# Performance work log

Hardware: AMD Instinct MI355X
Metric: run time of the kernel (lower is better)

The kernel has to match this reference:

```python
import jax, jax.numpy as jnp
import numpy as np

B, S, T = 1024, 1024, 16


def setup_inputs() -> dict:
    key = jax.random.key(0)
    k1, k2, k3, k4, k5 = jax.random.split(key, 5)
    emissions = jax.random.normal(k1, (B, S, T), dtype=jnp.float32)
    tags = jax.random.randint(k2, (B, S), 0, T, dtype=jnp.int64)
    mask = jnp.ones((B, S), dtype=bool)
    # parameters (original uses uniform(-0.1, 0.1) init)
    transitions = jax.random.uniform(k3, (T, T), minval=-0.1, maxval=0.1, dtype=jnp.float32)
    start_transitions = jax.random.uniform(k4, (T,), minval=-0.1, maxval=0.1, dtype=jnp.float32)
    end_transitions = jax.random.uniform(k5, (T,), minval=-0.1, maxval=0.1, dtype=jnp.float32)
    return {
        "emissions": emissions,
        "tags": tags,
        "mask": mask,
        "transitions": transitions,
        "start_transitions": start_transitions,
        "end_transitions": end_transitions,
    }


def _forward_algorithm(emissions, mask, transitions, start_transitions, end_transitions):
    # emissions: [B,S,T], mask: [B,S] bool -> log partition [B]
    score0 = start_transitions + emissions[:, 0]  # [B,T]

    def step(score, xs):
        em_t, m_t = xs  # em_t: [B,T], m_t: [B]
        # next[b,i,j] = score[b,i] + transitions[i,j] + em_t[b,j]
        nxt = score[:, :, None] + transitions[None, :, :] + em_t[:, None, :]
        nxt = jax.nn.logsumexp(nxt, axis=1)  # over previous tag i
        score = jnp.where(m_t[:, None], nxt, score)
        return score, None

    em_rest = jnp.swapaxes(emissions[:, 1:], 0, 1)  # [S-1,B,T]
    m_rest = jnp.swapaxes(mask[:, 1:], 0, 1)        # [S-1,B]
    score, _ = jax.lax.scan(step, score0, (em_rest, m_rest))
    score = score + end_transitions
    return jax.nn.logsumexp(score, axis=1)


def _score_sentence(emissions, tags, mask, transitions, start_transitions, end_transitions):
    # gold-path score, vectorized over time. [B]
    bidx = jnp.arange(emissions.shape[0])
    score = start_transitions[tags[:, 0]] + emissions[:, 0][bidx, tags[:, 0]]
    # per-step emission scores [B,S]
    emit = jnp.take_along_axis(emissions, tags[:, :, None], axis=2)[:, :, 0]
    # NOTE: faithful to original: transitions[tags[t], tags[t-1]]
    trans = transitions[tags[:, 1:], tags[:, :-1]]  # [B,S-1]
    m = mask[:, 1:].astype(emissions.dtype)
    score = score + jnp.sum((emit[:, 1:] + trans) * m, axis=1)
    last_idx = jnp.sum(mask.astype(jnp.int32), axis=1) - 1  # [B]
    last_tags = jnp.take_along_axis(tags, last_idx[:, None].astype(tags.dtype), axis=1)[:, 0]
    score = score + end_transitions[last_tags]
    return score


def reference(emissions, tags, mask, transitions, start_transitions, end_transitions):
    emissions = emissions.astype(jnp.float32)
    gold = _score_sentence(emissions, tags, mask, transitions, start_transitions, end_transitions)
    logZ = _forward_algorithm(emissions, mask, transitions, start_transitions, end_transitions)
    nll = logZ - gold
    return jnp.mean(nll)
```

## Files before the change

### kernel.cpp

```cpp
#include <hip/hip_runtime.h>
#include <stdint.h>


#define BB 1024
#define SS 1024
#define TT 16
#define WPB 8
#define TL  128
#define XS  68
#define MS  20
#define OFFLN2 3.29244911f

typedef float    f32x4 __attribute__((ext_vector_type(4)));
typedef float    f32x2 __attribute__((ext_vector_type(2)));
typedef int      i32x4 __attribute__((ext_vector_type(4)));
typedef short    s16x8 __attribute__((ext_vector_type(8)));
typedef uint32_t u32x4 __attribute__((ext_vector_type(4)));

__device__ __forceinline__ uint32_t pkt(float lo, float hi) {
    return __builtin_amdgcn_perm(__float_as_uint(hi), __float_as_uint(lo), 0x07060302u);
}

#define RESCALE(sd, sc) {                                                   \
        float mx_ = fmaxf(fmaxf(sd[0], sd[1]), fmaxf(sd[2], sd[3]));        \
        mx_ = fmaxf(mx_, __shfl_xor(mx_, 16, 64));                          \
        mx_ = fmaxf(mx_, __shfl_xor(mx_, 32, 64));                          \
        const int e_ = (int)(__float_as_uint(mx_) >> 23) - 127;             \
        const float sf_ = __uint_as_float((uint32_t)(127 - e_) << 23);      \
        sd[0] *= sf_; sd[1] *= sf_; sd[2] *= sf_; sd[3] *= sf_;             \
        sc += e_; }

__device__ __forceinline__ void run_chains(float* xt, const f32x2 e01, const f32x2 e23,
                                           const int q, const int m, const bool skip_first,
                                           f32x4& P, int& sc)
{
    const f32x4 zero = {0.f, 0.f, 0.f, 0.f};
    f32x4 sd0, sd1;
    sd0[0] = sd1[0] = (4*q + 0 == m) ? 1.f : 0.f;
    sd0[1] = sd1[1] = (4*q + 1 == m) ? 1.f : 0.f;
    sd0[2] = sd1[2] = (4*q + 2 == m) ? 1.f : 0.f;
    sd0[3] = sd1[3] = (4*q + 3 == m) ? 1.f : 0.f;
    u32x4 au0, au1, bu0, bu1;
    au0.z = au0.w = au1.z = au1.w = 0u;
    bu0.z = bu0.w = bu1.z = bu1.w = 0u;

    const float* xr0 = xt + m * XS;
    const float* xr1 = xr0 + 32;

    #pragma unroll
    for (int g = 0; g < 8; ++g) {
        const f32x4 c0 = *(const f32x4*)(xr0 + 4 * g);
        const f32x4 c1 = *(const f32x4*)(xr1 + 4 * g);
        #pragma unroll
        for (int i = 0; i < 4; ++i) {
            if (!(skip_first && g == 0 && i == 0)) {
                f32x2 xx; xx.x = c0[i]; xx.y = c0[i];
                const f32x2 a01 = xx * e01;
                const f32x2 a23 = xx * e23;
                au0.x = pkt(a01.x, a01.y); au0.y = pkt(a23.x, a23.y);
                bu0.x = pkt(sd0[0], sd0[1]); bu0.y = pkt(sd0[2], sd0[3]);
                sd0 = __builtin_amdgcn_mfma_f32_16x16x32_bf16(
                        __builtin_bit_cast(s16x8, au0), __builtin_bit_cast(s16x8, bu0),
                        zero, 0, 0, 0);
            }
            {
                f32x2 xx; xx.x = c1[i]; xx.y = c1[i];
                const f32x2 a01 = xx * e01;
                const f32x2 a23 = xx * e23;
                au1.x = pkt(a01.x, a01.y); au1.y = pkt(a23.x, a23.y);
                bu1.x = pkt(sd1[0], sd1[1]); bu1.y = pkt(sd1[2], sd1[3]);
                sd1 = __builtin_amdgcn_mfma_f32_16x16x32_bf16(
                        __builtin_bit_cast(s16x8, au1), __builtin_bit_cast(s16x8, bu1),
                        zero, 0, 0, 0);
            }
        }
    }

    xt[(4*q + 0) * TT + m] = sd1[0];
    xt[(4*q + 1) * TT + m] = sd1[1];
    xt[(4*q + 2) * TT + m] = sd1[2];
    xt[(4*q + 3) * TT + m] = sd1[3];
    const f32x4 at = *(const f32x4*)(xt + m * TT + 4 * q);
    au0.x = pkt(at.x, at.y);   au0.y = pkt(at.z, at.w);
    bu0.x = pkt(sd0[0], sd0[1]); bu0.y = pkt(sd0[2], sd0[3]);
    P = __builtin_amdgcn_mfma_f32_16x16x32_bf16(
            __builtin_bit_cast(s16x8, au0), __builtin_bit_cast(s16x8, bu0), zero, 0, 0, 0);
    sc = 0;
    RESCALE(P, sc);
}

__global__ __launch_bounds__(512, 8) void crf_fused(
        const float* __restrict__ em,
        const float* __restrict__ trans,
        const int*   __restrict__ tags,
        const float* __restrict__ startt,
        const float* __restrict__ endt,
        float* __restrict__ part)
{
    __shared__ __align__(16) float xbuf[WPB][TT * XS];
    __shared__ __align__(16) int   scb [WPB][16];
    __shared__ float gpart[WPB];

    const int w    = threadIdx.x >> 6;
    const int lane = threadIdx.x & 63;
    const int b    = blockIdx.x;
    const int q    = lane >> 4;
    const int m    = lane & 15;

    const float comp = 1.00390625f;
    f32x2 e01, e23;
    e01.x = __expf(trans[(4*q + 0) * TT + m]) * comp;
    e01.y = __expf(trans[(4*q + 1) * TT + m]) * comp;
    e23.x = __expf(trans[(4*q + 2) * TT + m]) * comp;
    e23.y = __expf(trans[(4*q + 3) * TT + m]) * comp;

    float* xt = xbuf[w];
    const float* ep = em + (size_t)b * SS * TT + (size_t)w * TL * TT + lane;

    {
        float v[16];
        #pragma unroll
        for (int k = 0; k < 16; ++k) v[k] = ep[k * 64];
        #pragma unroll
        for (int k = 0; k < 16; ++k) xt[m * XS + 4 * k + q] = __expf(v[k] - OFFLN2);
    }

    {
        const int t0  = w * TL + lane;
        const int t1  = t0 + 64;
        const int tg0 = tags[b * SS + t0];
        const int tg1 = tags[b * SS + t1];
        float g0 = em[((size_t)b * SS + t0) * TT + tg0];
        float g1 = em[((size_t)b * SS + t1) * TT + tg1];
        g0 += (t0 > 0) ? trans[tg0 * TT + tags[b * SS + t0 - 1]] : startt[tg0];
        g1 += trans[tg1 * TT + tags[b * SS + t1 - 1]];
        if (t1 == SS - 1) g1 += endt[tg1];
        float gs = g0 + g1;
        #pragma unroll
        for (int s2 = 1; s2 < 64; s2 <<= 1) gs += __shfl_xor(gs, s2, 64);
        if (lane == 0) gpart[w] = gs;
    }

    f32x4 PA; int scA;
    run_chains(xt, e01, e23, q, m, (w == 0), PA, scA);

    {
        float v[16];
        #pragma unroll
        for (int k = 0; k < 16; ++k) v[k] = ep[(16 + k) * 64];
        #pragma unroll
        for (int k = 0; k < 16; ++k) xt[m * XS + 4 * k + q] = __expf(v[k] - OFFLN2);
    }
    f32x4 PB; int scB;
    run_chains(xt, e01, e23, q, m, false, PB, scB);

    const f32x4 zero = {0.f, 0.f, 0.f, 0.f};
    xt[(4*q + 0) * TT + m] = PB[0];
    xt[(4*q + 1) * TT + m] = PB[1];
    xt[(4*q + 2) * TT + m] = PB[2];
    xt[(4*q + 3) * TT + m] = PB[3];
    const f32x4 at = *(const f32x4*)(xt + m * TT + 4 * q);
    u32x4 au, bu;
    au.z = au.w = bu.z = bu.w = 0u;
    au.x = pkt(at.x, at.y);   au.y = pkt(at.z, at.w);
    bu.x = pkt(PA[0], PA[1]); bu.y = pkt(PA[2], PA[3]);
    f32x4 sdw = __builtin_amdgcn_mfma_f32_16x16x32_bf16(
            __builtin_bit_cast(s16x8, au), __builtin_bit_cast(s16x8, bu), zero, 0, 0, 0);
    int scw = scA + scB;
    RESCALE(sdw, scw);

    xt[(4*q + 0) * MS + m] = sdw[0];
    xt[(4*q + 1) * MS + m] = sdw[1];
    xt[(4*q + 2) * MS + m] = sdw[2];
    xt[(4*q + 3) * MS + m] = sdw[3];
    if (q == 0) scb[w][m] = scw;
    __syncthreads();

    f32x4 d = zero; int sig = 0;
    #pragma unroll
    for (int lev = 0; lev < 3; ++lev) {
        const int nact = 4 >> lev;
        if (w < nact) {
            const int iA = (2 * w + 1) << lev;
            const int iB = (2 * w) << lev;
            const float* xA = xbuf[iA];
            float*       xB = xbuf[iB];
            const f32x4 a  = *(const f32x4*)(xA + m * MS + 4 * q);
            const i32x4 s4 = *(const i32x4*)(&scb[iA][4 * q]);
            const int   sB = scb[iB][m];
            int smax = max(max(s4.x, s4.y), max(s4.z, s4.w));
            smax = max(smax, __shfl_xor(smax, 16, 64));
            smax = max(smax, __shfl_xor(smax, 32, 64));
            const float bb0 = xB[(4*q + 0) * MS + m];
            const float bb1 = xB[(4*q + 1) * MS + m];
            const float bb2 = xB[(4*q + 2) * MS + m];
            const float bb3 = xB[(4*q + 3) * MS + m];
            const float u0 = ldexpf(bb0, s4.x - smax);
            const float u1 = ldexpf(bb1, s4.y - smax);
            const float u2 = ldexpf(bb2, s4.z - smax);
            const float u3 = ldexpf(bb3, s4.w - smax);
            u32x4 ta, tb;
            ta.z = ta.w = tb.z = tb.w = 0u;
            ta.x = pkt(a.x, a.y); ta.y = pkt(a.z, a.w);
            tb.x = pkt(u0, u1);   tb.y = pkt(u2, u3);
            f32x4 dd = __builtin_amdgcn_mfma_f32_16x16x32_bf16(
                    __builtin_bit_cast(s16x8, ta), __builtin_bit_cast(s16x8, tb), zero, 0, 0, 0);
            int sc_ = sB + smax;
            RESCALE(dd, sc_);
            if (lev == 2) { d = dd; sig = sc_; }
            else {
                xB[(4*q + 0) * MS + m] = dd[0];
                xB[(4*q + 1) * MS + m] = dd[1];
                xB[(4*q + 2) * MS + m] = dd[2];
                xB[(4*q + 3) * MS + m] = dd[3];
                if (q == 0) scb[iB][m] = sc_;
            }
        }
        if (lev < 2) __syncthreads();
    }

    if (w == 0) {
        const float s0 = startt[m] + em[(size_t)b * SS * TT + m];
        float mx0 = s0;
        #pragma unroll
        for (int s2 = 1; s2 < 16; s2 <<= 1) mx0 = fmaxf(mx0, __shfl_xor(mx0, s2, 64));
        const float u0n = __expf(s0 - mx0);
        int sigmax = sig;
        #pragma unroll
        for (int s2 = 1; s2 < 16; s2 <<= 1) sigmax = max(sigmax, __shfl_xor(sigmax, s2, 64));
        const float wt = ldexpf(u0n, sig - sigmax);
        f32x4 v;
        v[0] = d[0] * wt; v[1] = d[1] * wt; v[2] = d[2] * wt; v[3] = d[3] * wt;
        #pragma unroll
        for (int s2 = 1; s2 < 16; s2 <<= 1) {
            v[0] += __shfl_xor(v[0], s2, 64);
            v[1] += __shfl_xor(v[1], s2, 64);
            v[2] += __shfl_xor(v[2], s2, 64);
            v[3] += __shfl_xor(v[3], s2, 64);
        }
        const f32x4 ee = *(const f32x4*)(endt + 4 * q);
        float z = __expf(ee.x) * v[0] + __expf(ee.y) * v[1]
                + __expf(ee.z) * v[2] + __expf(ee.w) * v[3];
        z += __shfl_xor(z, 16, 64);
        z += __shfl_xor(z, 32, 64);
        if (lane == 0) {
            float gb = 0.f;
            #pragma unroll
            for (int i = 0; i < WPB; ++i) gb += gpart[i];
            part[b] = mx0 + 0.69314718055994531f * (float)sigmax
                    + 1023.0f * OFFLN2 + __logf(z) - gb;
        }
    }
}

__global__ __launch_bounds__(256) void reduce_kernel(const float* __restrict__ part,
                                                     float* __restrict__ out)
{
    __shared__ float red[256];
    const int tid = threadIdx.x;
    float s = 0.f;
    #pragma unroll
    for (int i = 0; i < 4; ++i) s += part[tid + 256 * i];
    red[tid] = s;
    __syncthreads();
    for (int k = 128; k > 0; k >>= 1) {
        if (tid < k) red[tid] += red[tid + k];
        __syncthreads();
    }
    if (tid == 0) out[0] = red[0] * (1.0f / BB);
}

extern "C" void kernel_launch(void* const* d_in, const int* in_sizes, int n_in,
                              void* d_out, int out_size, void* d_ws, size_t ws_size,
                              hipStream_t stream) {
    const float* em     = (const float*)d_in[0];
    const int*   tags   = (const int*)  d_in[1];
    const float* trans  = (const float*)d_in[3];
    const float* startt = (const float*)d_in[4];
    const float* endt   = (const float*)d_in[5];
    float* out  = (float*)d_out;
    float* part = (float*)d_ws;

    crf_fused<<<BB, 512, 0, stream>>>(em, trans, tags, startt, endt, part);
    reduce_kernel<<<1, 256, 0, stream>>>(part, out);
}
```

Before: 125.9 us.

## Use four parallel chains with constant MFMA A operand and post-multiply emissions

Restructures the per-warp chain product from two chains of 32 steps to four chains of 16 steps. The exp(transitions) A operand is packed once into a constant bf16 register instead of being rescaled and repacked by the emission column every step. Emissions are now applied by an elementwise multiply on the MFMA output, read from a transposed LDS layout. More independent chains hide MFMA latency, and the per-step packing work shrinks. The cost is two extra matrix merges per phase and a different LDS layout.

```diff
diff --git a/kernel.cpp b/kernel.cpp
--- a/kernel.cpp
+++ b/kernel.cpp
@@ -7,12 +7,10 @@
 #define TT 16
 #define WPB 8
 #define TL  128
-#define XS  68
 #define MS  20
 #define OFFLN2 3.29244911f
 
 typedef float    f32x4 __attribute__((ext_vector_type(4)));
-typedef float    f32x2 __attribute__((ext_vector_type(2)));
 typedef int      i32x4 __attribute__((ext_vector_type(4)));
 typedef short    s16x8 __attribute__((ext_vector_type(8)));
 typedef uint32_t u32x4 __attribute__((ext_vector_type(4)));
@@ -30,63 +28,59 @@
         sd[0] *= sf_; sd[1] *= sf_; sd[2] *= sf_; sd[3] *= sf_;             \
         sc += e_; }
 
-__device__ __forceinline__ void run_chains(float* xt, const f32x2 e01, const f32x2 e23,
-                                           const int q, const int m, const bool skip_first,
-                                           f32x4& P, int& sc)
+__device__ __forceinline__ f32x4 mmul(float* slot, const f32x4 L, const f32x4 R,
+                                      const int q, const int m) {
+    const f32x4 zero = {0.f, 0.f, 0.f, 0.f};
+    slot[(4*q + 0) * TT + m] = L[0];
+    slot[(4*q + 1) * TT + m] = L[1];
+    slot[(4*q + 2) * TT + m] = L[2];
+    slot[(4*q + 3) * TT + m] = L[3];
+    const f32x4 at = *(const f32x4*)(slot + m * TT + 4 * q);
+    u32x4 a, b;
+    a.z = a.w = b.z = b.w = 0u;
+    a.x = pkt(at.x, at.y); a.y = pkt(at.z, at.w);
+    b.x = pkt(R[0], R[1]); b.y = pkt(R[2], R[3]);
+    return __builtin_amdgcn_mfma_f32_16x16x32_bf16(
+            __builtin_bit_cast(s16x8, a), __builtin_bit_cast(s16x8, b), zero, 0, 0, 0);
+}
+
+__device__ __forceinline__ void run_phase(float* xt, const s16x8 eA,
+                                          const int q, const int m, const bool skip_first,
+                                          f32x4& P, int& sc)
 {
     const f32x4 zero = {0.f, 0.f, 0.f, 0.f};
-    f32x4 sd0, sd1;
-    sd0[0] = sd1[0] = (4*q + 0 == m) ? 1.f : 0.f;
-    sd0[1] = sd1[1] = (4*q + 1 == m) ? 1.f : 0.f;
-    sd0[2] = sd1[2] = (4*q + 2 == m) ? 1.f : 0.f;
-    sd0[3] = sd1[3] = (4*q + 3 == m) ? 1.f : 0.f;
-    u32x4 au0, au1, bu0, bu1;
-    au0.z = au0.w = au1.z = au1.w = 0u;
-    bu0.z = bu0.w = bu1.z = bu1.w = 0u;
-
-    const float* xr0 = xt + m * XS;
-    const float* xr1 = xr0 + 32;
-
-    #pragma unroll
-    for (int g = 0; g < 8; ++g) {
-        const f32x4 c0 = *(const f32x4*)(xr0 + 4 * g);
-        const f32x4 c1 = *(const f32x4*)(xr1 + 4 * g);
-        #pragma unroll
-        for (int i = 0; i < 4; ++i) {
-            if (!(skip_first && g == 0 && i == 0)) {
-                f32x2 xx; xx.x = c0[i]; xx.y = c0[i];
-                const f32x2 a01 = xx * e01;
-                const f32x2 a23 = xx * e23;
-                au0.x = pkt(a01.x, a01.y); au0.y = pkt(a23.x, a23.y);
-                bu0.x = pkt(sd0[0], sd0[1]); bu0.y = pkt(sd0[2], sd0[3]);
-                sd0 = __builtin_amdgcn_mfma_f32_16x16x32_bf16(
-                        __builtin_bit_cast(s16x8, au0), __builtin_bit_cast(s16x8, bu0),
-                        zero, 0, 0, 0);
-            }
-            {
-                f32x2 xx; xx.x = c1[i]; xx.y = c1[i];
-                const f32x2 a01 = xx * e01;
-                const f32x2 a23 = xx * e23;
-                au1.x = pkt(a01.x, a01.y); au1.y = pkt(a23.x, a23.y);
-                bu1.x = pkt(sd1[0], sd1[1]); bu1.y = pkt(sd1[2], sd1[3]);
-                sd1 = __builtin_amdgcn_mfma_f32_16x16x32_bf16(
-                        __builtin_bit_cast(s16x8, au1), __builtin_bit_cast(s16x8, bu1),
-                        zero, 0, 0, 0);
-            }
-        }
-    }
-
-    xt[(4*q + 0) * TT + m] = sd1[0];
-    xt[(4*q + 1) * TT + m] = sd1[1];
-    xt[(4*q + 2) * TT + m] = sd1[2];
-    xt[(4*q + 3) * TT + m] = sd1[3];
-    const f32x4 at = *(const f32x4*)(xt + m * TT + 4 * q);
-    au0.x = pkt(at.x, at.y);   au0.y = pkt(at.z, at.w);
-    bu0.x = pkt(sd0[0], sd0[1]); bu0.y = pkt(sd0[2], sd0[3]);
-    P = __builtin_amdgcn_mfma_f32_16x16x32_bf16(
-            __builtin_bit_cast(s16x8, au0), __builtin_bit_cast(s16x8, bu0), zero, 0, 0, 0);
+    f32x4 sd[4];
+    #pragma unroll
+    for (int c = 0; c < 4; ++c) {
+        sd[c][0] = (4*q + 0 == m) ? 1.f : 0.f;
+        sd[c][1] = (4*q + 1 == m) ? 1.f : 0.f;
+        sd[c][2] = (4*q + 2 == m) ? 1.f : 0.f;
+        sd[c][3] = (4*q + 3 == m) ? 1.f : 0.f;
+    }
+    u32x4 bu;
+    bu.z = bu.w = 0u;
+
+    const float* xr = xt + 4 * q;
+    #pragma unroll
+    for (int i = 0; i < 16; ++i) {
+        #pragma unroll
+        for (int c = 0; c < 4; ++c) {
+            if (skip_first && c == 0 && i == 0) continue;
+            const f32x4 x4 = *(const f32x4*)(xr + (16 * c + i) * TT);
+            bu.x = pkt(sd[c][0], sd[c][1]);
+            bu.y = pkt(sd[c][2], sd[c][3]);
+            const f32x4 dd = __builtin_amdgcn_mfma_f32_16x16x32_bf16(
+                    eA, __builtin_bit_cast(s16x8, bu), zero, 0, 0, 0);
+            sd[c] = dd * x4;
+        }
+    }
+
+    const f32x4 p01 = mmul(xt,       sd[1], sd[0], q, m);
+    const f32x4 p23 = mmul(xt + 256, sd[3], sd[2], q, m);
+    f32x4 pp        = mmul(xt + 512, p23,   p01,   q, m);
     sc = 0;
-    RESCALE(P, sc);
+    RESCALE(pp, sc);
+    P = pp;
 }
 
 __global__ __launch_bounds__(512, 8) void crf_fused(
@@ -97,7 +91,7 @@
         const float* __restrict__ endt,
         float* __restrict__ part)
 {
-    __shared__ __align__(16) float xbuf[WPB][TT * XS];
+    __shared__ __align__(16) float xbuf[WPB][64 * TT];
     __shared__ __align__(16) int   scb [WPB][16];
     __shared__ float gpart[WPB];
 
@@ -108,11 +102,15 @@
     const int m    = lane & 15;
 
     const float comp = 1.00390625f;
-    f32x2 e01, e23;
-    e01.x = __expf(trans[(4*q + 0) * TT + m]) * comp;
-    e01.y = __expf(trans[(4*q + 1) * TT + m]) * comp;
-    e23.x = __expf(trans[(4*q + 2) * TT + m]) * comp;
-    e23.y = __expf(trans[(4*q + 3) * TT + m]) * comp;
+    u32x4 ea;
+    {
+        const float e0 = __expf(trans[(4*q + 0) * TT + m]) * comp;
+        const float e1 = __expf(trans[(4*q + 1) * TT + m]) * comp;
+        const float e2 = __expf(trans[(4*q + 2) * TT + m]) * comp;
+        const float e3 = __expf(trans[(4*q + 3) * TT + m]) * comp;
+        ea.x = pkt(e0, e1); ea.y = pkt(e2, e3); ea.z = ea.w = 0u;
+    }
+    const s16x8 eA = __builtin_bit_cast(s16x8, ea);
 
     float* xt = xbuf[w];
     const float* ep = em + (size_t)b * SS * TT + (size_t)w * TL * TT + lane;
@@ -122,7 +120,7 @@
         #pragma unroll
         for (int k = 0; k < 16; ++k) v[k] = ep[k * 64];
         #pragma unroll
-        for (int k = 0; k < 16; ++k) xt[m * XS + 4 * k + q] = __expf(v[k] - OFFLN2);
+        for (int k = 0; k < 16; ++k) xt[(4 * k + q) * TT + m] = __expf(v[k] - OFFLN2);
     }
 
     {
@@ -142,30 +140,19 @@
     }
 
     f32x4 PA; int scA;
-    run_chains(xt, e01, e23, q, m, (w == 0), PA, scA);
+    run_phase(xt, eA, q, m, (w == 0), PA, scA);
 
     {
         float v[16];
         #pragma unroll
         for (int k = 0; k < 16; ++k) v[k] = ep[(16 + k) * 64];
         #pragma unroll
-        for (int k = 0; k < 16; ++k) xt[m * XS + 4 * k + q] = __expf(v[k] - OFFLN2);
+        for (int k = 0; k < 16; ++k) xt[(4 * k + q) * TT + m] = __expf(v[k] - OFFLN2);
     }
     f32x4 PB; int scB;
-    run_chains(xt, e01, e23, q, m, false, PB, scB);
-
-    const f32x4 zero = {0.f, 0.f, 0.f, 0.f};
-    xt[(4*q + 0) * TT + m] = PB[0];
-    xt[(4*q + 1) * TT + m] = PB[1];
-    xt[(4*q + 2) * TT + m] = PB[2];
-    xt[(4*q + 3) * TT + m] = PB[3];
-    const f32x4 at = *(const f32x4*)(xt + m * TT + 4 * q);
-    u32x4 au, bu;
-    au.z = au.w = bu.z = bu.w = 0u;
-    au.x = pkt(at.x, at.y);   au.y = pkt(at.z, at.w);
-    bu.x = pkt(PA[0], PA[1]); bu.y = pkt(PA[2], PA[3]);
-    f32x4 sdw = __builtin_amdgcn_mfma_f32_16x16x32_bf16(
-            __builtin_bit_cast(s16x8, au), __builtin_bit_cast(s16x8, bu), zero, 0, 0, 0);
+    run_phase(xt, eA, q, m, false, PB, scB);
+
+    f32x4 sdw = mmul(xt + 512, PB, PA, q, m);
     int scw = scA + scB;
     RESCALE(sdw, scw);
 
@@ -176,6 +163,7 @@
     if (q == 0) scb[w][m] = scw;
     __syncthreads();
 
+    const f32x4 zero = {0.f, 0.f, 0.f, 0.f};
     f32x4 d = zero; int sig = 0;
     #pragma unroll
     for (int lev = 0; lev < 3; ++lev) {
```

Result: faster. 120.4 us (-4.4%).
